# Performance work log

Hardware: AMD Instinct MI355X
Metric: run time of the kernel (lower is better)

Reference implementation:

```python
import jax, jax.numpy as jnp
import numpy as np

B, S, D, H = 2, 4096, 128, 128
EPS = 1e-6
NEG_INF = -1e30


def _complex_linear(xr, xi, Wr, Wi, br, bi):
    # x: (B,S,D); W: (H,D); complex linear (Wr + i Wi)(xr + i xi) + (br + i bi) per layer math:
    # real_out = (xr Wr + br) - (xi Wi + bi); imag_out = (xi Wr + br) + (xr Wi + bi)
    out_r = xr @ Wr.T + br - (xi @ Wi.T + bi)
    out_i = xi @ Wr.T + br + (xr @ Wi.T + bi)
    return out_r, out_i


def setup_inputs() -> dict:
    key = jax.random.key(0)
    ks = jax.random.split(key, 24)
    scale = 1.0 / np.sqrt(D)
    def W(k):
        return jax.random.normal(k, (H, D), jnp.float32) * scale
    def b(k):
        return jax.random.normal(k, (H,), jnp.float32) * 0.01
    inp = {
        "Z_q": jax.random.normal(ks[0], (B, 2, S, D, 1), jnp.float32),
        "Z_k": jax.random.normal(ks[1], (B, 2, S, D, 1), jnp.float32),
        "Z_v": jax.random.normal(ks[2], (B, 2, S, D, 1), jnp.float32),
        "Wq_r": W(ks[3]), "Wq_i": W(ks[4]), "bq_r": b(ks[5]), "bq_i": b(ks[6]),
        "Wk_r": W(ks[7]), "Wk_i": W(ks[8]), "bk_r": b(ks[9]), "bk_i": b(ks[10]),
        "Wv_r": W(ks[11]), "Wv_i": W(ks[12]), "bv_r": b(ks[13]), "bv_i": b(ks[14]),
        "Wp_r": W(ks[15]), "Wp_i": W(ks[16]), "bp_r": b(ks[17]), "bp_i": b(ks[18]),
        "noise_floor": jnp.asarray(1.0, jnp.float32),
        "tau": jnp.asarray(0.0, jnp.float32),
    }
    return inp


def reference(Z_q, Z_k, Z_v,
              Wq_r, Wq_i, bq_r, bq_i,
              Wk_r, Wk_i, bk_r, bk_i,
              Wv_r, Wv_i, bv_r, bv_i,
              Wp_r, Wp_i, bp_r, bp_i,
              noise_floor, tau):
    # squeeze trailing singleton; split real/imag -> (B,S,D)
    zqr, zqi = Z_q[:, 0, :, :, 0], Z_q[:, 1, :, :, 0]
    zkr, zki = Z_k[:, 0, :, :, 0], Z_k[:, 1, :, :, 0]
    zvr, zvi = Z_v[:, 0, :, :, 0], Z_v[:, 1, :, :, 0]

    Qr, Qi = _complex_linear(zqr, zqi, Wq_r, Wq_i, bq_r, bq_i)
    Kr, Ki = _complex_linear(zkr, zki, Wk_r, Wk_i, bk_r, bk_i)
    Vr, Vi = _complex_linear(zvr, zvi, Wv_r, Wv_i, bv_r, bv_i)

    # InverseMahalanobis: R2[b,i,j] = sum_h |Q[b,i]-K[b,j]|^2
    q2 = jnp.sum(Qr * Qr + Qi * Qi, axis=-1)          # (B,S)
    k2 = jnp.sum(Kr * Kr + Ki * Ki, axis=-1)          # (B,S)
    re_qk = (jnp.einsum('bsh,bth->bst', Qr, Kr)
             + jnp.einsum('bsh,bth->bst', Qi, Ki))    # (B,S,S)
    R2 = q2[:, :, None] + k2[:, None, :] - 2.0 * re_qk

    attn_scores = -jax.nn.softplus(tau) * jnp.log(noise_floor ** 2 + R2 + EPS)
    mask = jnp.tril(jnp.ones((S, S), dtype=bool))[None]
    attn_scores = jnp.where(mask, attn_scores, NEG_INF)
    attn_weights = jax.nn.softmax(attn_scores / jnp.sqrt(jnp.float32(H)), axis=-1)

    # attn (real) times complex V
    est_r = jnp.einsum('bst,bth->bsh', attn_weights, Vr)
    est_i = jnp.einsum('bst,bth->bsh', attn_weights, Vi)

    out_r, out_i = _complex_linear(est_r, est_i, Wp_r, Wp_i, bp_r, bp_i)
    out = jnp.stack((out_r, out_i), axis=1)[..., None]  # (B,2,S,H,1)
    return out, attn_weights
```

## Files before the change

kernel.cpp:

```cpp
#include <hip/hip_runtime.h>

#define S_LEN 4096
#define NBATCH 2
#define OUT_ELEMS 2097152

typedef _Float16 f16;
typedef _Float16 f16x8 __attribute__((ext_vector_type(8)));
typedef _Float16 f16x4 __attribute__((ext_vector_type(4)));
typedef float f32x4 __attribute__((ext_vector_type(4)));

#define MT_OFF    0x000000
#define BIAS_OFF  0x080000
#define SC_OFF    0x081000
#define QH_OFF    0x100000
#define KH_OFF    0x500000
#define VH_OFF    0x900000
#define Q2_OFF    0xD00000
#define K2_OFF    0xD10000
#define L_OFF     0xD20000
#define VPT_OFF   0xE00000
#define PW_OFF    0x1600000
#define WS_NEED   0x5600000

#define MFMA16(A,B,C) __builtin_amdgcn_mfma_f32_16x16x32_f16(A,B,C,0,0,0)

__device__ __forceinline__ void async_cp16(f16* lds, const f16* g) {
  __builtin_amdgcn_global_load_lds(
      (const __attribute__((address_space(1))) void*)g,
      (__attribute__((address_space(3))) void*)lds, 16, 0, 0);
}


__device__ __forceinline__ void stage16(f16* lds, const f16* g, int stride, int tid) {
#pragma unroll
  for (int i = 0; i < 2; ++i) {
    int idx = i*256 + tid;
    int row = idx >> 2, c = idx & 3;
    int cs = c ^ ((row >> 1) & 3);
    async_cp16(lds + idx*8, g + (size_t)row*stride + cs*8);
  }
}

__device__ __forceinline__ void stage32(f16* lds, const float* g, int stride, int tid) {
#pragma unroll
  for (int i = 0; i < 4; ++i) {
    int idx = i*256 + tid;
    int row = idx >> 3, c = idx & 7;
    const float4* gp = (const float4*)(g + (size_t)row*stride + c*4);
    float4 v = *gp;
    f16x4 h; h[0]=(f16)v.x; h[1]=(f16)v.y; h[2]=(f16)v.z; h[3]=(f16)v.w;
    int cl = (((c >> 1) ^ ((row >> 1) & 3)) << 1) | (c & 1);
    *(f16x4*)(lds + row*32 + cl*4) = h;
  }
}

__device__ __forceinline__ void mfma_step(const f16* Asm, const f16* Bsm, int lane,
                                          int wm, int wn, f32x4 acc[4][4]) {
  f16x8 a[4], b[4];
  int rr = lane & 15;
  int sc = (lane >> 4) ^ ((rr >> 1) & 3);
#pragma unroll
  for (int i=0;i<4;i++) a[i] = *(const f16x8*)(Asm + (wm + i*16 + rr)*32 + (sc<<3));
#pragma unroll
  for (int j=0;j<4;j++) b[j] = *(const f16x8*)(Bsm + (wn + j*16 + rr)*32 + (sc<<3));
#pragma unroll
  for (int i=0;i<4;i++)
#pragma unroll
    for (int j=0;j<4;j++) acc[i][j] = MFMA16(a[i], b[j], acc[i][j]);
}

__global__ __launch_bounds__(256)
void k_build(const float* Wqr, const float* Wqi, const float* bqr, const float* bqi,
             const float* Wkr, const float* Wki, const float* bkr, const float* bki,
             const float* Wvr, const float* Wvi, const float* bvr, const float* bvi,
             const float* Wpr, const float* Wpi, const float* bpr, const float* bpi,
             f16* Mt, float* bias) {
  int mat = blockIdx.x;
  const float *Wr, *Wi, *br, *bi;
  if (mat == 0)      { Wr=Wqr; Wi=Wqi; br=bqr; bi=bqi; }
  else if (mat == 1) { Wr=Wkr; Wi=Wki; br=bkr; bi=bki; }
  else if (mat == 2) { Wr=Wvr; Wi=Wvi; br=bvr; bi=bvi; }
  else               { Wr=Wpr; Wi=Wpi; br=bpr; bi=bpi; }
  int idx = blockIdx.y*256 + threadIdx.x;
  int n = idx >> 8, k = idx & 255;
  int d = k & 127, h = n & 127;
  float w = (k < 128) ? ((n < 128) ? Wr[h*128+d] : Wi[h*128+d])
                      : ((n < 128) ? -Wi[h*128+d] : Wr[h*128+d]);
  Mt[mat*65536 + n*256 + k] = (f16)w;
  if (k == 0)
    bias[mat*256 + n] = (n < 128) ? (br[n] - bi[n]) : (br[n-128] + bi[n-128]);
}

__global__ __launch_bounds__(256)
void k_init(float* outp, float* zreg, float* sc, const float* bias,
            const float* nf, const float* tau) {
  int idx = blockIdx.x*256 + threadIdx.x;
  if (idx < 1048576) {
    int hq = idx & 31;
    int comp = (idx >> 17) & 1;
    ((float4*)outp)[idx] = *(const float4*)(bias + 3*256 + comp*128 + hq*4);
  } else {
    int j = idx - 1048576;
    if (j < 12288) ((float4*)zreg)[j] = make_float4(0.f,0.f,0.f,0.f);
  }
  if (idx == 0) {
    float t = tau[0];
    float c = __builtin_log2f(1.0f + __builtin_exp2f(t * 1.4426950408889634f))
              * 0.6931471805599453f;
    sc[0] = -c * 0.08838834764831845f;
    sc[1] = nf[0]*nf[0] + 1e-6f;
  }
}

__global__ __launch_bounds__(256)
void k_proj(const float* Zq, const float* Zk, const float* Zv,
            const f16* Mt, const float* bias,
            f16* Qh, f16* Kh, f16* Vh, float* q2, float* k2) {
  __shared__ f16 Asm[2][128*32];
  __shared__ f16 Bsm[2][128*32];
  __shared__ float bias_s[128];
  int tid = threadIdx.x;
  int mode = blockIdx.z;
  int m0 = blockIdx.x * 128, n0 = blockIdx.y * 128;
  const float* Z = (mode==0) ? Zq : (mode==1 ? Zk : Zv);
  const f16* Bt = Mt + mode*65536;
  if (tid < 128) bias_s[tid] = bias[mode*256 + n0 + tid];
  int b = m0 >> 12, s0 = m0 & 4095;
  int lane = tid & 63, w = tid >> 6;
  int wm = (w >> 1)*64, wn = (w & 1)*64;
  f32x4 acc[4][4] = {};
  {
    const float* Ag = Z + (((size_t)(b*2 + 0))*S_LEN + s0)*128 + 0;
    stage32(Asm[0], Ag, 128, tid);
    stage16(Bsm[0], Bt + n0*256 + 0, 256, tid);
  }
  __syncthreads();
  for (int kb = 0; kb < 8; ++kb) {
    int cur = kb & 1;
    if (kb < 7) {
      int k1 = (kb+1)*32;
      int part = k1 >> 7, d0 = k1 & 127;
      const float* Ag = Z + (((size_t)(b*2 + part))*S_LEN + s0)*128 + d0;
      stage32(Asm[cur^1], Ag, 128, tid);
      stage16(Bsm[cur^1], Bt + n0*256 + k1, 256, tid);
    }
    mfma_step(Asm[cur], Bsm[cur], lane, wm, wn, acc);
    __syncthreads();
  }
  int rr = (lane>>4)*4, cc = lane & 15;
  f16* O = (mode==0) ? Qh : (mode==1 ? Kh : Vh);
  float rs[4][4];
#pragma unroll
  for (int i=0;i<4;i++)
#pragma unroll
    for (int r=0;r<4;r++) rs[i][r]=0.f;
#pragma unroll
  for (int i=0;i<4;i++)
#pragma unroll
    for (int j=0;j<4;j++) {
      int cl = wn + j*16 + cc;
      int cg = n0 + cl;
      float bv = bias_s[cl];
#pragma unroll
      for (int r=0;r<4;r++) {
        int rg = m0 + wm + i*16 + rr + r;
        f16 hv = (f16)(acc[i][j][r] + bv);
        O[(size_t)rg*256 + cg] = hv;
        float fv = (float)hv;
        rs[i][r] += fv*fv;
      }
    }
  if (mode < 2) {
#pragma unroll
    for (int m=8;m>=1;m>>=1)
#pragma unroll
      for (int i=0;i<4;i++)
#pragma unroll
        for (int r=0;r<4;r++) rs[i][r] += __shfl_xor(rs[i][r], m, 64);
    if (cc == 0) {
      float* T = (mode==0) ? q2 : k2;
#pragma unroll
      for (int i=0;i<4;i++)
#pragma unroll
        for (int r=0;r<4;r++) {
          int rg = m0 + wm + i*16 + rr + r;
          atomicAdd(&T[rg], rs[i][r]);
        }
    }
  }
}

__global__ __launch_bounds__(256)
void k_vp(const f16* Vh, const f16* Mt, f16* VPt) {
  __shared__ f16 Asm[2][128*32];
  __shared__ f16 Bsm[2][128*32];
  int t0 = blockIdx.x*128, n0 = blockIdx.y*128, b = blockIdx.z;
  int tid = threadIdx.x;
  int lane = tid & 63, w = tid >> 6;
  int wm = (w>>1)*64, wn = (w&1)*64;
  const f16* Ag = Mt + 3*65536 + n0*256;
  const f16* Bg = Vh + ((size_t)(b*S_LEN) + t0)*256;
  f32x4 acc[4][4] = {};
  stage16(Asm[0], Ag, 256, tid);
  stage16(Bsm[0], Bg, 256, tid);
  __syncthreads();
  for (int kb=0;kb<8;kb++) {
    int cur = kb & 1;
    if (kb < 7) {
      stage16(Asm[cur^1], Ag + (kb+1)*32, 256, tid);
      stage16(Bsm[cur^1], Bg + (kb+1)*32, 256, tid);
    }
    mfma_step(Asm[cur], Bsm[cur], lane, wm, wn, acc);
    __syncthreads();
  }
  int rr = (lane>>4)*4, cc = lane & 15;
#pragma unroll
  for (int i=0;i<4;i++) {
    int n = n0 + wm + i*16 + rr;
#pragma unroll
    for (int j=0;j<4;j++) {
      int t = t0 + wn + j*16 + cc;
#pragma unroll
      for (int r=0;r<4;r++)
        VPt[(size_t)b*1048576 + (size_t)(n + r)*4096 + t] = (f16)acc[i][j][r];
    }
  }
}

__global__ __launch_bounds__(256)
void k_attn(const f16* Qh, const f16* Kh, const float* q2, const float* k2,
            const float* sc, float* lsum, f16* Pws, float* attn) {
  int x = blockIdx.x;
  int b = x >> 10, r = x & 1023;
  int sb = r >> 5, tb = r & 31;
  int s0 = sb*128, t0 = tb*128;
  int tid = threadIdx.x;
  if (tb > sb) {
    float4 z = make_float4(0.f,0.f,0.f,0.f);
    int row = tid >> 1, h = tid & 1;
    float4* p = (float4*)(attn + ((size_t)(b*S_LEN) + s0 + row)*S_LEN + t0 + h*64);
#pragma unroll
    for (int i=0;i<16;i++) p[i] = z;
    return;
  }
  __shared__ f16 Asm[2][128*32];
  __shared__ f16 Bsm[2][128*32];
  __shared__ float q2s[128], k2s[128];
  if (tid < 128) {
    q2s[tid] = q2[b*S_LEN + s0 + tid];
    k2s[tid] = k2[b*S_LEN + t0 + tid];
  }
  float kc = sc[0], nf2 = sc[1];
  int lane = tid & 63, w = tid >> 6;
  int wm = (w >> 1)*64, wn = (w & 1)*64;
  const f16* Ag = Qh + ((size_t)(b*S_LEN) + s0)*256;
  const f16* Bg = Kh + ((size_t)(b*S_LEN) + t0)*256;
  f32x4 acc[4][4] = {};
  stage16(Asm[0], Ag, 256, tid);
  stage16(Bsm[0], Bg, 256, tid);
  __syncthreads();
  for (int kb=0;kb<8;kb++) {
    int cur = kb & 1;
    if (kb < 7) {
      stage16(Asm[cur^1], Ag + (kb+1)*32, 256, tid);
      stage16(Bsm[cur^1], Bg + (kb+1)*32, 256, tid);
    }
    mfma_step(Asm[cur], Bsm[cur], lane, wm, wn, acc);
    __syncthreads();
  }
  int rr = (lane>>4)*4, cc = lane & 15;
  bool diag = (tb == sb);
  float rs[4][4];
#pragma unroll
  for (int i=0;i<4;i++)
#pragma unroll
    for (int rg=0;rg<4;rg++) rs[i][rg]=0.f;
#pragma unroll
  for (int i=0;i<4;i++)
#pragma unroll
    for (int j=0;j<4;j++) {
      int cl = wn + j*16 + cc;
      float kv = k2s[cl];
#pragma unroll
      for (int rg=0;rg<4;rg++) {
        int rl = wm + i*16 + rr + rg;
        float xx = nf2 + q2s[rl] + kv - 2.0f*acc[i][j][rg];
        float P = __builtin_exp2f(kc * __builtin_log2f(__builtin_fmaxf(xx, 1e-6f)));
        if (diag && (t0+cl) > (s0+rl)) P = 0.f;
        Pws[((size_t)(b*S_LEN) + s0 + rl)*S_LEN + t0 + cl] = (f16)P;
        rs[i][rg] += P;
      }
    }
#pragma unroll
  for (int m=8;m>=1;m>>=1)
#pragma unroll
    for (int i=0;i<4;i++)
#pragma unroll
      for (int rg=0;rg<4;rg++) rs[i][rg] += __shfl_xor(rs[i][rg], m, 64);
  if (cc == 0)
#pragma unroll
    for (int i=0;i<4;i++)
#pragma unroll
      for (int rg=0;rg<4;rg++) {
        int rl = wm + i*16 + rr + rg;
        atomicAdd(&lsum[b*S_LEN + s0 + rl], rs[i][rg]);
      }
}

__global__ __launch_bounds__(256)
void k_pv(const f16* Pws, const f16* VPt, const float* lsum, float* outp, float* attn) {
  __shared__ f16 Asm[2][128*32];
  __shared__ f16 Bsm[2][128*32];
  __shared__ float ls[128];
  int r = blockIdx.x;
  int nb = blockIdx.y, b = blockIdx.z;
  int sb = 0;
  while (r >= ((sb+4)>>2)) { r -= (sb+4)>>2; sb++; }
  int c = r;
  int s0 = sb*128, h0 = nb*128;
  int tid = threadIdx.x;
  bool wrb = (nb == 0);
  if (tid < 128) ls[tid] = 1.0f / lsum[b*S_LEN + s0 + tid];
  int lane = tid & 63, w = tid >> 6;
  int wm = (w>>1)*64, wn = (w&1)*64;
  int tb0 = c*4, tb1 = tb0 + 4; if (tb1 > sb+1) tb1 = sb+1;
  int nt = (tb1 - tb0) * 4;
  int base_t = tb0*128;
  const f16* Abase = Pws + ((size_t)(b*S_LEN) + s0)*S_LEN + base_t;
  const f16* Bbase = VPt + (size_t)b*1048576 + (size_t)h0*4096 + base_t;
  f32x4 acc[4][4] = {};
  int row2 = tid >> 1, half2 = tid & 1;
  int xs2 = (row2 >> 1) & 3;
  stage16(Asm[0], Abase, S_LEN, tid);
  stage16(Bsm[0], Bbase, 4096, tid);
  __syncthreads();
  for (int st = 0; st < nt; ++st) {
    int cur = st & 1;
    int t0 = base_t + st*32;
    if (st + 1 < nt) {
      stage16(Asm[cur^1], Abase + (st+1)*32, S_LEN, tid);
      stage16(Bsm[cur^1], Bbase + (st+1)*32, 4096, tid);
    }
    if (wrb) {
      float invl = ls[row2];
      const f16* Arow = Asm[cur] + row2*32;
      f16x8 v0 = *(const f16x8*)(Arow + (((2*half2  ) ^ xs2) << 3));
      f16x8 v1 = *(const f16x8*)(Arow + (((2*half2+1) ^ xs2) << 3));
      float4* dst = (float4*)(attn + ((size_t)(b*S_LEN) + s0 + row2)*S_LEN + t0 + half2*16);
      float4 o;
      o.x=(float)v0[0]*invl; o.y=(float)v0[1]*invl; o.z=(float)v0[2]*invl; o.w=(float)v0[3]*invl; dst[0]=o;
      o.x=(float)v0[4]*invl; o.y=(float)v0[5]*invl; o.z=(float)v0[6]*invl; o.w=(float)v0[7]*invl; dst[1]=o;
      o.x=(float)v1[0]*invl; o.y=(float)v1[1]*invl; o.z=(float)v1[2]*invl; o.w=(float)v1[3]*invl; dst[2]=o;
      o.x=(float)v1[4]*invl; o.y=(float)v1[5]*invl; o.z=(float)v1[6]*invl; o.w=(float)v1[7]*invl; dst[3]=o;
    }
    mfma_step(Asm[cur], Bsm[cur], lane, wm, wn, acc);
    __syncthreads();
  }
  int rr = (lane>>4)*4, cc = lane & 15;
#pragma unroll
  for (int i=0;i<4;i++)
#pragma unroll
    for (int j=0;j<4;j++) {
      int cg = h0 + wn + j*16 + cc;
      int comp = cg >> 7, h = cg & 127;
#pragma unroll
      for (int rg=0;rg<4;rg++) {
        int rl = wm + i*16 + rr + rg;
        float v = acc[i][j][rg] * ls[rl];
        atomicAdd(&outp[(((size_t)(b*2 + comp))*S_LEN + s0 + rl)*128 + h], v);
      }
    }
}

extern "C" void kernel_launch(void* const* d_in, const int* in_sizes, int n_in,
                              void* d_out, int out_size, void* d_ws, size_t ws_size,
                              hipStream_t stream) {
  (void)in_sizes; (void)n_in; (void)out_size;
  if (ws_size < (size_t)WS_NEED) return;
  const float* Zq = (const float*)d_in[0];
  const float* Zk = (const float*)d_in[1];
  const float* Zv = (const float*)d_in[2];
  char* ws = (char*)d_ws;
  f16*   Mt   = (f16*)(ws + MT_OFF);
  float* bias = (float*)(ws + BIAS_OFF);
  float* sc   = (float*)(ws + SC_OFF);
  f16*   Qh   = (f16*)(ws + QH_OFF);
  f16*   Kh   = (f16*)(ws + KH_OFF);
  f16*   Vh   = (f16*)(ws + VH_OFF);
  float* q2   = (float*)(ws + Q2_OFF);
  float* k2   = (float*)(ws + K2_OFF);
  float* lsum = (float*)(ws + L_OFF);
  f16*   VPt  = (f16*)(ws + VPT_OFF);
  f16*   Pws  = (f16*)(ws + PW_OFF);
  float* outp = (float*)d_out;
  float* attn = outp + OUT_ELEMS;

  k_build<<<dim3(4,256), 256, 0, stream>>>(
      (const float*)d_in[3],  (const float*)d_in[4],  (const float*)d_in[5],  (const float*)d_in[6],
      (const float*)d_in[7],  (const float*)d_in[8],  (const float*)d_in[9],  (const float*)d_in[10],
      (const float*)d_in[11], (const float*)d_in[12], (const float*)d_in[13], (const float*)d_in[14],
      (const float*)d_in[15], (const float*)d_in[16], (const float*)d_in[17], (const float*)d_in[18],
      Mt, bias);
  k_init<<<4144, 256, 0, stream>>>(outp, q2, sc, bias, (const float*)d_in[19], (const float*)d_in[20]);
  k_proj<<<dim3(64,2,3), 256, 0, stream>>>(Zq, Zk, Zv, Mt, bias, Qh, Kh, Vh, q2, k2);
  k_vp<<<dim3(32,2,2), 256, 0, stream>>>(Vh, Mt, VPt);
  k_attn<<<2048, 256, 0, stream>>>(Qh, Kh, q2, k2, sc, lsum, Pws, attn);
  k_pv<<<dim3(144,2,2), 256, 0, stream>>>(Pws, VPt, lsum, outp, attn);
}
```

Baseline: 318.2 us.

## Stage P tiles through LDS, launch only lower-triangular attention tiles, zero upper tiles in init

The attention kernel now launches only the 528 causal (lower-triangular) tiles per batch, using a triangular index decode. Zero-filling the upper-triangular attn tiles moves into k_init. The P tile is written to shared memory first and then copied to global with 16-byte vector stores, replacing scattered 2-byte stores. k_init also shrinks the bias fill of the output to its actual size, where the old launch wrote about twice that many elements into the attn region. Costs are an extra barrier, LDS traffic in k_attn, and small serial loops to decode tile indices.

After: 310.1 us. 1.03x faster.

```diff
diff --git a/kernel.cpp b/kernel.cpp
--- a/kernel.cpp
+++ b/kernel.cpp
@@ -92,16 +92,31 @@
 }
 
 __global__ __launch_bounds__(256)
-void k_init(float* outp, float* zreg, float* sc, const float* bias,
+void k_init(float* outp, float* attn, float* zreg, float* sc, const float* bias,
             const float* nf, const float* tau) {
-  int idx = blockIdx.x*256 + threadIdx.x;
-  if (idx < 1048576) {
-    int hq = idx & 31;
+  int bx = blockIdx.x, tid = threadIdx.x;
+  float4 z = make_float4(0.f,0.f,0.f,0.f);
+  if (bx < 992) {
+    int b = bx >= 496; int r = bx - b*496;
+    int tb = 1; while (r >= tb) { r -= tb; tb++; }
+    int sb = r;
+    float* base = attn + ((size_t)(b*S_LEN) + sb*128)*S_LEN + tb*128;
+    int c4 = tid & 31;
+#pragma unroll
+    for (int it = 0; it < 16; ++it) {
+      int row = it*8 + (tid >> 5);
+      *(float4*)(base + (size_t)row*S_LEN + c4*4) = z;
+    }
+    return;
+  }
+  int idx = (bx - 992)*256 + tid;
+  if (idx < 524288) {
+    int h4 = idx & 31;
     int comp = (idx >> 17) & 1;
-    ((float4*)outp)[idx] = *(const float4*)(bias + 3*256 + comp*128 + hq*4);
+    ((float4*)outp)[idx] = *(const float4*)(bias + 3*256 + comp*128 + h4*4);
   } else {
-    int j = idx - 1048576;
-    if (j < 12288) ((float4*)zreg)[j] = make_float4(0.f,0.f,0.f,0.f);
+    int j = idx - 524288;
+    if (j < 12288) ((float4*)zreg)[j] = z;
   }
   if (idx == 0) {
     float t = tau[0];
@@ -229,23 +244,19 @@
 
 __global__ __launch_bounds__(256)
 void k_attn(const f16* Qh, const f16* Kh, const float* q2, const float* k2,
-            const float* sc, float* lsum, f16* Pws, float* attn) {
+            const float* sc, float* lsum, f16* Pws) {
+  __shared__ f16 smem[4*128*32];
+  __shared__ float q2s[128], k2s[128];
+  f16* Asm0 = smem;
+  f16* Asm1 = smem + 4096;
+  f16* Bsm0 = smem + 8192;
+  f16* Bsm1 = smem + 12288;
   int x = blockIdx.x;
-  int b = x >> 10, r = x & 1023;
-  int sb = r >> 5, tb = r & 31;
+  int b = x >= 528; int r = x - b*528;
+  int sb = 0; while (r > sb) { r -= sb + 1; sb++; }
+  int tb = r;
   int s0 = sb*128, t0 = tb*128;
   int tid = threadIdx.x;
-  if (tb > sb) {
-    float4 z = make_float4(0.f,0.f,0.f,0.f);
-    int row = tid >> 1, h = tid & 1;
-    float4* p = (float4*)(attn + ((size_t)(b*S_LEN) + s0 + row)*S_LEN + t0 + h*64);
-#pragma unroll
-    for (int i=0;i<16;i++) p[i] = z;
-    return;
-  }
-  __shared__ f16 Asm[2][128*32];
-  __shared__ f16 Bsm[2][128*32];
-  __shared__ float q2s[128], k2s[128];
   if (tid < 128) {
     q2s[tid] = q2[b*S_LEN + s0 + tid];
     k2s[tid] = k2[b*S_LEN + t0 + tid];
@@ -256,18 +267,19 @@
   const f16* Ag = Qh + ((size_t)(b*S_LEN) + s0)*256;
   const f16* Bg = Kh + ((size_t)(b*S_LEN) + t0)*256;
   f32x4 acc[4][4] = {};
-  stage16(Asm[0], Ag, 256, tid);
-  stage16(Bsm[0], Bg, 256, tid);
+  stage16(Asm0, Ag, 256, tid);
+  stage16(Bsm0, Bg, 256, tid);
   __syncthreads();
   for (int kb=0;kb<8;kb++) {
     int cur = kb & 1;
     if (kb < 7) {
-      stage16(Asm[cur^1], Ag + (kb+1)*32, 256, tid);
-      stage16(Bsm[cur^1], Bg + (kb+1)*32, 256, tid);
-    }
-    mfma_step(Asm[cur], Bsm[cur], lane, wm, wn, acc);
+      stage16(cur ? Asm0 : Asm1, Ag + (kb+1)*32, 256, tid);
+      stage16(cur ? Bsm0 : Bsm1, Bg + (kb+1)*32, 256, tid);
+    }
+    mfma_step(cur ? Asm1 : Asm0, cur ? Bsm1 : Bsm0, lane, wm, wn, acc);
     __syncthreads();
   }
+  f16* Psm = smem;
   int rr = (lane>>4)*4, cc = lane & 15;
   bool diag = (tb == sb);
   float rs[4][4];
@@ -287,10 +299,18 @@
         float xx = nf2 + q2s[rl] + kv - 2.0f*acc[i][j][rg];
         float P = __builtin_exp2f(kc * __builtin_log2f(__builtin_fmaxf(xx, 1e-6f)));
         if (diag && (t0+cl) > (s0+rl)) P = 0.f;
-        Pws[((size_t)(b*S_LEN) + s0 + rl)*S_LEN + t0 + cl] = (f16)P;
+        Psm[rl*128 + cl] = (f16)P;
         rs[i][rg] += P;
       }
     }
+  __syncthreads();
+  f16* Pg = Pws + ((size_t)(b*S_LEN) + s0)*S_LEN + t0;
+#pragma unroll
+  for (int i2 = 0; i2 < 8; ++i2) {
+    int idx = i2*256 + tid;
+    int row = idx >> 4, c = idx & 15;
+    *(f16x8*)(Pg + (size_t)row*S_LEN + c*8) = *(const f16x8*)(Psm + row*128 + c*8);
+  }
 #pragma unroll
   for (int m=8;m>=1;m>>=1)
 #pragma unroll
@@ -401,9 +421,10 @@
       (const float*)d_in[11], (const float*)d_in[12], (const float*)d_in[13], (const float*)d_in[14],
       (const float*)d_in[15], (const float*)d_in[16], (const float*)d_in[17], (const float*)d_in[18],
       Mt, bias);
-  k_init<<<4144, 256, 0, stream>>>(outp, q2, sc, bias, (const float*)d_in[19], (const float*)d_in[20]);
+  k_init<<<3088, 256, 0, stream>>>(outp, attn, q2, sc, bias,
+                                   (const float*)d_in[19], (const float*)d_in[20]);
   k_proj<<<dim3(64,2,3), 256, 0, stream>>>(Zq, Zk, Zv, Mt, bias, Qh, Kh, Vh, q2, k2);
   k_vp<<<dim3(32,2,2), 256, 0, stream>>>(Vh, Mt, VPt);
-  k_attn<<<2048, 256, 0, stream>>>(Qh, Kh, q2, k2, sc, lsum, Pws, attn);
+  k_attn<<<1056, 256, 0, stream>>>(Qh, Kh, q2, k2, sc, lsum, Pws);
   k_pv<<<dim3(144,2,2), 256, 0, stream>>>(Pws, VPt, lsum, outp, attn);
 }
```
